# Optimization experiments

Measured on AMD Instinct MI355X. Metric: run time of the kernel, lower is better.

## Reference

```python
import jax, jax.numpy as jnp
import numpy as np

H_DIM = 4096
N_HEADS = 4
D_HEAD = H_DIM // N_HEADS  # 1024; also forced to equal the node count N
N = D_HEAD
LN_EPS = 1e-5


def setup_inputs() -> dict:
    key = jax.random.key(0)
    ks = jax.random.split(key, 10)
    s = 0.02
    return {
        "node1": jax.random.normal(ks[0], (N, H_DIM), dtype=jnp.float32),
        "node2": jax.random.normal(ks[1], (N, H_DIM), dtype=jnp.float32),
        # stacked per-head projection weights (torch Linear y = x @ W^T + b; here W stored as [h, in, out])
        "Wq": jax.random.normal(ks[2], (N_HEADS, H_DIM, D_HEAD), dtype=jnp.float32) * s,
        "bq": jax.random.normal(ks[3], (N_HEADS, D_HEAD), dtype=jnp.float32) * s,
        "Wk": jax.random.normal(ks[4], (N_HEADS, H_DIM, D_HEAD), dtype=jnp.float32) * s,
        "bk": jax.random.normal(ks[5], (N_HEADS, D_HEAD), dtype=jnp.float32) * s,
        "Wv": jax.random.normal(ks[6], (N_HEADS, H_DIM, D_HEAD), dtype=jnp.float32) * s,
        "bv": jax.random.normal(ks[7], (N_HEADS, D_HEAD), dtype=jnp.float32) * s,
        "gamma": jnp.ones((H_DIM,), dtype=jnp.float32),
        "beta": jnp.zeros((H_DIM,), dtype=jnp.float32),
    }


def reference(node1, node2, Wq, bq, Wk, bk, Wv, bv, gamma, beta):
    # per-head projections: [h, N, d]
    q = jnp.einsum('nd,hdf->hnf', node1, Wq) + bq[:, None, :]
    k = jnp.einsum('md,hdf->hmf', node2, Wk) + bk[:, None, :]
    v = jnp.einsum('md,hdf->hmf', node2, Wv) + bv[:, None, :]
    scale = 1.0 / jnp.sqrt(jnp.asarray(D_HEAD, dtype=q.dtype))
    # scores [h, N, N]; elementwise-multiplied by v (no softmax). Valid because N == D_HEAD.
    r = (jnp.einsum('hnf,hmf->hnm', q, k) * scale) * v
    # concat heads along last dim: [N, h * d] = [N, H_DIM]
    out = jnp.transpose(r, (1, 0, 2)).reshape(N, H_DIM)
    # LayerNorm over last dim (biased variance, matching torch)
    mu = jnp.mean(out, axis=-1, keepdims=True)
    var = jnp.mean((out - mu) ** 2, axis=-1, keepdims=True)
    return (out - mu) * jax.lax.rsqrt(var + LN_EPS) * gamma + beta
```

## Files before the change

### kernel.cpp

```cpp
#include <hip/hip_runtime.h>

#define H_DIM 4096
#define DH 1024
#define NROWS 1024

typedef __attribute__((ext_vector_type(8))) short short8;
typedef __attribute__((ext_vector_type(4))) short short4v;
typedef __attribute__((ext_vector_type(4))) float f32x4;

#define AS_GLOBAL __attribute__((address_space(1)))
#define AS_LDS __attribute__((address_space(3)))

__device__ __forceinline__ short f2bf(float f) {
  union { float f; unsigned u; } v; v.f = f;
  unsigned r = v.u + 0x7fffu + ((v.u >> 16) & 1u);
  return (short)(r >> 16);
}
__device__ __forceinline__ float bf2f(short s) {
  union { unsigned u; float f; } v;
  v.u = ((unsigned)(unsigned short)s) << 16;
  return v.f;
}

__device__ __forceinline__ void gload16(const void* g, void* l) {
  __builtin_amdgcn_global_load_lds((const AS_GLOBAL void*)g, (AS_LDS void*)l, 16, 0, 0);
}

__device__ __forceinline__ void stage_tile(const short* Xrow0, size_t rowstride, int kbase,
                                           short* lds, int t) {
  const int w = t >> 6;
#pragma unroll
  for (int p = 0; p < 2; ++p) {
    const short* g = Xrow0 + (size_t)(p * 64 + (t >> 2)) * rowstride + kbase + (t & 3) * 8;
    char* l = (char*)lds + p * 4096 + w * 1024;
    gload16(g, l);
  }
}

__global__ void convert_nodes(const float* __restrict__ n1, const float* __restrict__ n2,
                              short* __restrict__ o1, short* __restrict__ o2) {
  const float* src = blockIdx.y ? n2 : n1;
  short* dst = blockIdx.y ? o2 : o1;
  const size_t i = ((size_t)blockIdx.x * 256 + threadIdx.x) * 8;
  f32x4 a = *(const f32x4*)&src[i];
  f32x4 b = *(const f32x4*)&src[i + 4];
  short8 s;
  s[0] = f2bf(a.x); s[1] = f2bf(a.y); s[2] = f2bf(a.z); s[3] = f2bf(a.w);
  s[4] = f2bf(b.x); s[5] = f2bf(b.y); s[6] = f2bf(b.z); s[7] = f2bf(b.w);
  *(short8*)&dst[i] = s;
}

__global__ void convert_w_t(const float* __restrict__ W, short* __restrict__ Wt) {
  __shared__ short tile[64][72];
  const int h = blockIdx.z, dt = blockIdx.y, ft = blockIdx.x;
  const float* Wh = W + (size_t)h * H_DIM * DH;
  short* Wth = Wt + (size_t)h * DH * H_DIM;
  const int t = threadIdx.x;
  {
    const int d = t >> 2, f0 = (t & 3) * 16;
    const float* src = Wh + (size_t)(dt * 64 + d) * DH + ft * 64 + f0;
    f32x4 v0 = *(const f32x4*)(src + 0);
    f32x4 v1 = *(const f32x4*)(src + 4);
    f32x4 v2 = *(const f32x4*)(src + 8);
    f32x4 v3 = *(const f32x4*)(src + 12);
    short8 s0, s1;
    s0[0] = f2bf(v0.x); s0[1] = f2bf(v0.y); s0[2] = f2bf(v0.z); s0[3] = f2bf(v0.w);
    s0[4] = f2bf(v1.x); s0[5] = f2bf(v1.y); s0[6] = f2bf(v1.z); s0[7] = f2bf(v1.w);
    s1[0] = f2bf(v2.x); s1[1] = f2bf(v2.y); s1[2] = f2bf(v2.z); s1[3] = f2bf(v2.w);
    s1[4] = f2bf(v3.x); s1[5] = f2bf(v3.y); s1[6] = f2bf(v3.z); s1[7] = f2bf(v3.w);
    *(short8*)&tile[d][f0] = s0;
    *(short8*)&tile[d][f0 + 8] = s1;
  }
  __syncthreads();
  {
    const int f = t >> 2, d0 = (t & 3) * 16;
    short8 o0, o1;
#pragma unroll
    for (int j = 0; j < 8; ++j) o0[j] = tile[d0 + j][f];
#pragma unroll
    for (int j = 0; j < 8; ++j) o1[j] = tile[d0 + 8 + j][f];
    short* dst = Wth + (size_t)(ft * 64 + f) * H_DIM + dt * 64 + d0;
    *(short8*)(dst) = o0;
    *(short8*)(dst + 8) = o1;
  }
}

__launch_bounds__(256)
__global__ void qkv_bt(const short* __restrict__ n1b, const short* __restrict__ n2b,
                       const short* __restrict__ Wt,
                       const float* __restrict__ bq, const float* __restrict__ bk,
                       const float* __restrict__ bv,
                       short* __restrict__ qkv_out, int g0) {
  const int bid = blockIdx.x;
  const int gl = bid >> 6;
  const int gg = g0 + gl;
  const int tile = bid & 63;
  const short* A = (gg < 4) ? n1b : n2b;
  const short* B = Wt + (size_t)gl * NROWS * H_DIM;
  const float* bias = ((gg < 4) ? bq : (gg < 8) ? bk : bv) + (gg & 3) * DH;
  short* C = qkv_out + (size_t)gg * NROWS * DH;
  const int bm0 = (tile >> 3) * 128, bn0 = (tile & 7) * 128;

  __shared__ short As[2][4096];
  __shared__ short Bs[2][4096];

  const int t = threadIdx.x;
  const int lane = t & 63, w = t >> 6;
  const int wm = (w >> 1) * 64, wn = (w & 1) * 64;
  const int lr = lane & 15, lk = lane >> 4;

  const short* Arow0 = A + (size_t)bm0 * H_DIM;
  const short* Brow0 = B + (size_t)bn0 * H_DIM;

  f32x4 acc[4][4];
#pragma unroll
  for (int m = 0; m < 4; ++m)
#pragma unroll
    for (int n = 0; n < 4; ++n)
      acc[m][n] = (f32x4)(0.0f);

  stage_tile(Arow0, H_DIM, 0, &As[0][0], t);
  stage_tile(Brow0, H_DIM, 0, &Bs[0][0], t);
  __syncthreads();

  const int NKT = H_DIM / 32;
  int cur = 0;
  for (int kt = 0; kt < NKT; ++kt) {
    if (kt + 1 < NKT) {
      stage_tile(Arow0, H_DIM, (kt + 1) * 32, &As[cur ^ 1][0], t);
      stage_tile(Brow0, H_DIM, (kt + 1) * 32, &Bs[cur ^ 1][0], t);
    }
    short8 af[4], bf_[4];
#pragma unroll
    for (int m = 0; m < 4; ++m)
      af[m] = *(const short8*)((const char*)&As[cur][0] + (wm + m * 16 + lr) * 64 + lk * 16);
#pragma unroll
    for (int n = 0; n < 4; ++n)
      bf_[n] = *(const short8*)((const char*)&Bs[cur][0] + (wn + n * 16 + lr) * 64 + lk * 16);
#pragma unroll
    for (int m = 0; m < 4; ++m)
#pragma unroll
      for (int n = 0; n < 4; ++n)
        acc[m][n] = __builtin_amdgcn_mfma_f32_16x16x32_bf16(af[m], bf_[n], acc[m][n], 0, 0, 0);
    __syncthreads();
    cur ^= 1;
  }

#pragma unroll
  for (int n = 0; n < 4; ++n) {
    const int col = bn0 + wn + n * 16 + lr;
    const float bv_ = bias[col];
#pragma unroll
    for (int m = 0; m < 4; ++m) {
      const int row0 = bm0 + wm + m * 16 + lk * 4;
#pragma unroll
      for (int r = 0; r < 4; ++r)
        C[(size_t)(row0 + r) * DH + col] = f2bf(acc[m][n][r] + bv_);
    }
  }
}

__launch_bounds__(256)
__global__ void attn_bt(const short* __restrict__ qkv, float* __restrict__ out) {
  const int bid = blockIdx.x;
  const int h = bid >> 6;
  const int tile = bid & 63;
  const short* Q = qkv + (size_t)h * NROWS * DH;
  const short* K = qkv + (size_t)(4 + h) * NROWS * DH;
  const short* V = qkv + (size_t)(8 + h) * NROWS * DH;
  const int bm0 = (tile >> 3) * 128, bn0 = (tile & 7) * 128;

  __shared__ short As[2][4096];
  __shared__ short Bs[2][4096];

  const int t = threadIdx.x;
  const int lane = t & 63, w = t >> 6;
  const int wm = (w >> 1) * 64, wn = (w & 1) * 64;
  const int lr = lane & 15, lk = lane >> 4;

  const short* Arow0 = Q + (size_t)bm0 * DH;
  const short* Brow0 = K + (size_t)bn0 * DH;

  f32x4 acc[4][4];
#pragma unroll
  for (int m = 0; m < 4; ++m)
#pragma unroll
    for (int n = 0; n < 4; ++n)
      acc[m][n] = (f32x4)(0.0f);

  stage_tile(Arow0, DH, 0, &As[0][0], t);
  stage_tile(Brow0, DH, 0, &Bs[0][0], t);
  __syncthreads();

  const int NKT = DH / 32;
  int cur = 0;
  for (int kt = 0; kt < NKT; ++kt) {
    if (kt + 1 < NKT) {
      stage_tile(Arow0, DH, (kt + 1) * 32, &As[cur ^ 1][0], t);
      stage_tile(Brow0, DH, (kt + 1) * 32, &Bs[cur ^ 1][0], t);
    }
    short8 af[4], bf_[4];
#pragma unroll
    for (int m = 0; m < 4; ++m)
      af[m] = *(const short8*)((const char*)&As[cur][0] + (wm + m * 16 + lr) * 64 + lk * 16);
#pragma unroll
    for (int n = 0; n < 4; ++n)
      bf_[n] = *(const short8*)((const char*)&Bs[cur][0] + (wn + n * 16 + lr) * 64 + lk * 16);
#pragma unroll
    for (int m = 0; m < 4; ++m)
#pragma unroll
      for (int n = 0; n < 4; ++n)
        acc[m][n] = __builtin_amdgcn_mfma_f32_16x16x32_bf16(af[m], bf_[n], acc[m][n], 0, 0, 0);
    __syncthreads();
    cur ^= 1;
  }

  const float scale = 0.03125f;
#pragma unroll
  for (int n = 0; n < 4; ++n) {
    const int col = bn0 + wn + n * 16 + lr;
#pragma unroll
    for (int m = 0; m < 4; ++m) {
      const int row0 = bm0 + wm + m * 16 + lk * 4;
#pragma unroll
      for (int r = 0; r < 4; ++r) {
        const int row = row0 + r;
        const float vv = bf2f(V[(size_t)row * DH + col]);
        out[(size_t)row * H_DIM + h * DH + col] = acc[m][n][r] * scale * vv;
      }
    }
  }
}

__launch_bounds__(256, 2)
__global__ void qkv_gemm(const float* __restrict__ node1,
                         const float* __restrict__ node2,
                         const float* __restrict__ Wq, const float* __restrict__ bq,
                         const float* __restrict__ Wk, const float* __restrict__ bk,
                         const float* __restrict__ Wv, const float* __restrict__ bv,
                         short* __restrict__ qkv_out) {
  const int gid = blockIdx.x;
  const int gemm = gid >> 6;
  const int tile = gid & 63;
  const int qkv = gemm >> 2;
  const int h = gemm & 3;
  const float* A = (qkv == 0) ? node1 : node2;
  const float* W = (qkv == 0) ? Wq : (qkv == 1 ? Wk : Wv);
  const float* bias = (qkv == 0) ? bq : (qkv == 1 ? bk : bv);
  const float* B = W + (size_t)h * H_DIM * DH;
  const float* bh = bias + h * DH;
  short* C = qkv_out + (size_t)gemm * NROWS * DH;
  const int bm0 = (tile >> 3) * 128;
  const int bn0 = (tile & 7) * 128;
  __shared__ short As[128][40];
  __shared__ short Bs[128][40];
  const int t = threadIdx.x;
  const int lane = t & 63;
  const int w = t >> 6;
  const int wm = (w >> 1) * 64;
  const int wn = (w & 1) * 64;
  const int lr = lane & 15;
  const int lk = lane >> 4;
  const int ar = t >> 3;
  const int ac = (t & 7) * 4;
  const int bfc = t & 127;
  const int bd = (t >> 7) * 16;
  f32x4 acc[4][4];
#pragma unroll
  for (int m = 0; m < 4; ++m)
#pragma unroll
    for (int n = 0; n < 4; ++n)
      acc[m][n] = (f32x4)(0.0f);
  f32x4 rA[4];
  float rB[16];
  const float* Abase = A + (size_t)bm0 * H_DIM;
  const float* Bbase = B + bn0 + bfc;
#pragma unroll
  for (int p = 0; p < 4; ++p)
    rA[p] = *(const f32x4*)&Abase[(size_t)(ar + 32 * p) * H_DIM + ac];
#pragma unroll
  for (int i = 0; i < 16; ++i)
    rB[i] = Bbase[(size_t)(bd + i) * DH];
  const int NKT = H_DIM / 32;
  for (int kt = 0; kt < NKT; ++kt) {
    __syncthreads();
#pragma unroll
    for (int p = 0; p < 4; ++p) {
      short4v s;
      s.x = f2bf(rA[p].x); s.y = f2bf(rA[p].y);
      s.z = f2bf(rA[p].z); s.w = f2bf(rA[p].w);
      *(short4v*)&As[ar + 32 * p][ac] = s;
    }
    {
      short8 lo, hi;
#pragma unroll
      for (int i = 0; i < 8; ++i) { lo[i] = f2bf(rB[i]); hi[i] = f2bf(rB[8 + i]); }
      *(short8*)&Bs[bfc][bd] = lo;
      *(short8*)&Bs[bfc][bd + 8] = hi;
    }
    __syncthreads();
    if (kt + 1 < NKT) {
      const int k0 = (kt + 1) * 32;
#pragma unroll
      for (int p = 0; p < 4; ++p)
        rA[p] = *(const f32x4*)&Abase[(size_t)(ar + 32 * p) * H_DIM + k0 + ac];
#pragma unroll
      for (int i = 0; i < 16; ++i)
        rB[i] = Bbase[(size_t)(k0 + bd + i) * DH];
    }
    short8 af[4], bf_[4];
#pragma unroll
    for (int m = 0; m < 4; ++m)
      af[m] = *(const short8*)&As[wm + m * 16 + lr][lk * 8];
#pragma unroll
    for (int n = 0; n < 4; ++n)
      bf_[n] = *(const short8*)&Bs[wn + n * 16 + lr][lk * 8];
#pragma unroll
    for (int m = 0; m < 4; ++m)
#pragma unroll
      for (int n = 0; n < 4; ++n)
        acc[m][n] = __builtin_amdgcn_mfma_f32_16x16x32_bf16(af[m], bf_[n], acc[m][n], 0, 0, 0);
  }
#pragma unroll
  for (int n = 0; n < 4; ++n) {
    const int col = bn0 + wn + n * 16 + lr;
    const float bv_ = bh[col];
#pragma unroll
    for (int m = 0; m < 4; ++m) {
      const int row0 = bm0 + wm + m * 16 + lk * 4;
#pragma unroll
      for (int r = 0; r < 4; ++r)
        C[(size_t)(row0 + r) * DH + col] = f2bf(acc[m][n][r] + bv_);
    }
  }
}

__launch_bounds__(256, 4)
__global__ void ln_kernel(float* __restrict__ out, const float* __restrict__ gamma,
                          const float* __restrict__ beta) {
  const int row = blockIdx.x;
  const int t = threadIdx.x;
  float* p = out + (size_t)row * H_DIM;
  f32x4 x[4];
  float s1 = 0.f, s2 = 0.f;
#pragma unroll
  for (int i = 0; i < 4; ++i) {
    x[i] = *(const f32x4*)&p[t * 4 + i * 1024];
    s1 += x[i].x + x[i].y + x[i].z + x[i].w;
    s2 += x[i].x * x[i].x + x[i].y * x[i].y + x[i].z * x[i].z + x[i].w * x[i].w;
  }
#pragma unroll
  for (int o = 32; o > 0; o >>= 1) {
    s1 += __shfl_down(s1, o);
    s2 += __shfl_down(s2, o);
  }
  __shared__ float w1[4], w2[4];
  if ((t & 63) == 0) { w1[t >> 6] = s1; w2[t >> 6] = s2; }
  __syncthreads();
  const float tot1 = w1[0] + w1[1] + w1[2] + w1[3];
  const float tot2 = w2[0] + w2[1] + w2[2] + w2[3];
  const float mu = tot1 * (1.0f / H_DIM);
  const float var = tot2 * (1.0f / H_DIM) - mu * mu;
  const float rs = rsqrtf(var + 1e-5f);
#pragma unroll
  for (int i = 0; i < 4; ++i) {
    const int c = t * 4 + i * 1024;
    const f32x4 g = *(const f32x4*)&gamma[c];
    const f32x4 b = *(const f32x4*)&beta[c];
    f32x4 y;
    y.x = (x[i].x - mu) * rs * g.x + b.x;
    y.y = (x[i].y - mu) * rs * g.y + b.y;
    y.z = (x[i].z - mu) * rs * g.z + b.z;
    y.w = (x[i].w - mu) * rs * g.w + b.w;
    *(f32x4*)&p[c] = y;
  }
}

extern "C" void kernel_launch(void* const* d_in, const int* in_sizes, int n_in,
                              void* d_out, int out_size, void* d_ws, size_t ws_size,
                              hipStream_t stream) {
  const float* node1 = (const float*)d_in[0];
  const float* node2 = (const float*)d_in[1];
  const float* Wq = (const float*)d_in[2];
  const float* bq = (const float*)d_in[3];
  const float* Wk = (const float*)d_in[4];
  const float* bk = (const float*)d_in[5];
  const float* Wv = (const float*)d_in[6];
  const float* bv = (const float*)d_in[7];
  const float* gamma = (const float*)d_in[8];
  const float* beta = (const float*)d_in[9];
  float* out = (float*)d_out;

  const size_t MB = (size_t)1 << 20;
  short* qkv = (short*)d_ws;
  short* n1b = qkv + ((size_t)12 << 20);
  short* n2b = n1b + ((size_t)4 << 20);
  short* Wt = qkv + ((size_t)20 << 20);

  if (ws_size >= 136 * MB) {
    convert_nodes<<<dim3(2048, 2), 256, 0, stream>>>(node1, node2, n1b, n2b);
    convert_w_t<<<dim3(16, 64, 4), 256, 0, stream>>>(Wq, Wt);
    convert_w_t<<<dim3(16, 64, 4), 256, 0, stream>>>(Wk, Wt + ((size_t)16 << 20));
    convert_w_t<<<dim3(16, 64, 4), 256, 0, stream>>>(Wv, Wt + ((size_t)32 << 20));
    qkv_bt<<<768, 256, 0, stream>>>(n1b, n2b, Wt, bq, bk, bv, qkv, 0);
  } else if (ws_size >= 72 * MB) {
    convert_nodes<<<dim3(2048, 2), 256, 0, stream>>>(node1, node2, n1b, n2b);
    const float* Ws[3] = {Wq, Wk, Wv};
    for (int s = 0; s < 3; ++s) {
      convert_w_t<<<dim3(16, 64, 4), 256, 0, stream>>>(Ws[s], Wt);
      qkv_bt<<<256, 256, 0, stream>>>(n1b, n2b, Wt, bq, bk, bv, qkv, s * 4);
    }
  } else {
    qkv_gemm<<<768, 256, 0, stream>>>(node1, node2, Wq, bq, Wk, bk, Wv, bv, qkv);
  }

  attn_bt<<<256, 256, 0, stream>>>(qkv, out);
  ln_kernel<<<1024, 256, 0, stream>>>(out, gamma, beta);
}
```

Measured before the change: 237.6 us.

## Replace QKV GEMM with 256x256-tile 8-wave pipelined kernel using swizzled LDS

Replaces the 128x128-tile QKV projection GEMM with a kernel using 256x256 output tiles, 8 waves, and a BK=64 double-buffered LDS pipeline. LDS is XOR-swizzled, loads are interleaved with MFMA phases using barriers and s_setprio, and blocks are remapped across GEMMs. The aim is to raise arithmetic intensity per LDS byte and hide global load latency. It also drops the mid-workspace fallback path, so that size range now takes the slow fp32 GEMM, and 192 blocks of 512 threads may underfill the GPU's CUs.

```diff
diff --git a/kernel.cpp b/kernel.cpp
--- a/kernel.cpp
+++ b/kernel.cpp
@@ -24,17 +24,6 @@
 
 __device__ __forceinline__ void gload16(const void* g, void* l) {
   __builtin_amdgcn_global_load_lds((const AS_GLOBAL void*)g, (AS_LDS void*)l, 16, 0, 0);
-}
-
-__device__ __forceinline__ void stage_tile(const short* Xrow0, size_t rowstride, int kbase,
-                                           short* lds, int t) {
-  const int w = t >> 6;
-#pragma unroll
-  for (int p = 0; p < 2; ++p) {
-    const short* g = Xrow0 + (size_t)(p * 64 + (t >> 2)) * rowstride + kbase + (t & 3) * 8;
-    char* l = (char*)lds + p * 4096 + w * 1024;
-    gload16(g, l);
-  }
 }
 
 __global__ void convert_nodes(const float* __restrict__ n1, const float* __restrict__ n2,
@@ -85,78 +74,142 @@
   }
 }
 
-__launch_bounds__(256)
-__global__ void qkv_bt(const short* __restrict__ n1b, const short* __restrict__ n2b,
+
+#define BAR __builtin_amdgcn_s_barrier();
+#define WAITL { asm volatile("s_waitcnt lgkmcnt(0)" ::: "memory"); __builtin_amdgcn_sched_barrier(0); }
+#define PRIO1 __builtin_amdgcn_s_setprio(1);
+#define PRIO0 __builtin_amdgcn_s_setprio(0);
+
+#define STG(isA, slab, ktn) \
+  gload16(((isA) ? Ag : Bg) + (size_t)(slab) * 64 * H_DIM + (ktn) * 64, \
+          smb + ((isA) ? 0 : 65536) + ((ktn) & 1) * 32768 + (slab) * 8192 + wub)
+
+#define DSA(mh, cbuf) { _Pragma("unroll") for (int mp = 0; mp < 4; ++mp) { \
+    const int rrow = wm * 128 + (mh) * 64 + mp * 16 + lr; \
+    const char* pb = smb + (cbuf) * 32768 + rrow * 128; \
+    af[mp * 2 + 0] = *(const short8*)(pb + sA0); \
+    af[mp * 2 + 1] = *(const short8*)(pb + sA1); } }
+
+#define DSB(nh, cbuf, dst) { _Pragma("unroll") for (int np = 0; np < 2; ++np) { \
+    const int brow = wn * 64 + (nh) * 32 + np * 16 + lr; \
+    const char* pb = smb + 65536 + (cbuf) * 32768 + brow * 128; \
+    dst[np * 2 + 0] = *(const short8*)(pb + sA0); \
+    dst[np * 2 + 1] = *(const short8*)(pb + sA1); } }
+
+#define MFMA16(mh, nh, bfr) { _Pragma("unroll") for (int mp = 0; mp < 4; ++mp) \
+    { _Pragma("unroll") for (int np = 0; np < 2; ++np) { \
+      acc[(mh) * 4 + mp][(nh) * 2 + np] = __builtin_amdgcn_mfma_f32_16x16x32_bf16( \
+          af[mp * 2 + 0], bfr[np * 2 + 0], acc[(mh) * 4 + mp][(nh) * 2 + np], 0, 0, 0); \
+      acc[(mh) * 4 + mp][(nh) * 2 + np] = __builtin_amdgcn_mfma_f32_16x16x32_bf16( \
+          af[mp * 2 + 1], bfr[np * 2 + 1], acc[(mh) * 4 + mp][(nh) * 2 + np], 0, 0, 0); } } }
+
+__launch_bounds__(512, 2)
+__global__ void qkv_8p(const short* __restrict__ n1b, const short* __restrict__ n2b,
                        const short* __restrict__ Wt,
                        const float* __restrict__ bq, const float* __restrict__ bk,
                        const float* __restrict__ bv,
-                       short* __restrict__ qkv_out, int g0) {
+                       short* __restrict__ qkv_out) {
+  __shared__ short smem[65536];
+  char* smb = (char*)smem;
+
   const int bid = blockIdx.x;
-  const int gl = bid >> 6;
-  const int gg = g0 + gl;
-  const int tile = bid & 63;
-  const short* A = (gg < 4) ? n1b : n2b;
-  const short* B = Wt + (size_t)gl * NROWS * H_DIM;
-  const float* bias = ((gg < 4) ? bq : (gg < 8) ? bk : bv) + (gg & 3) * DH;
-  short* C = qkv_out + (size_t)gg * NROWS * DH;
-  const int bm0 = (tile >> 3) * 128, bn0 = (tile & 7) * 128;
-
-  __shared__ short As[2][4096];
-  __shared__ short Bs[2][4096];
+  const int v = (bid & 7) * 24 + (bid >> 3);
+  const int gemm = v >> 4;
+  const int rr = v & 15;
+  const int mt = rr & 3, nt = rr >> 2;
+  const int bm0 = mt * 256, bn0 = nt * 256;
+  const short* A = (gemm < 4) ? n1b : n2b;
+  const short* B = Wt + ((size_t)gemm << 22);
+  const float* bias = ((gemm < 4) ? bq : (gemm < 8) ? bk : bv) + (gemm & 3) * DH;
+  short* C = qkv_out + ((size_t)gemm << 20);
 
   const int t = threadIdx.x;
   const int lane = t & 63, w = t >> 6;
-  const int wm = (w >> 1) * 64, wn = (w & 1) * 64;
+  const int wm = w >> 2, wn = w & 3;
   const int lr = lane & 15, lk = lane >> 4;
-
-  const short* Arow0 = A + (size_t)bm0 * H_DIM;
-  const short* Brow0 = B + (size_t)bn0 * H_DIM;
-
-  f32x4 acc[4][4];
-#pragma unroll
-  for (int m = 0; m < 4; ++m)
+  const int xorv = lr & 7;
+  const int sA0 = (lk ^ xorv) * 16;
+  const int sA1 = ((4 + lk) ^ xorv) * 16;
+
+  const int rowA = t >> 3;
+  const int sL = (t & 7) ^ (rowA & 7);
+  const size_t wub = (size_t)w * 1024;
+  const short* Ag = A + (size_t)(bm0 + rowA) * H_DIM + sL * 8;
+  const short* Bg = B + (size_t)(bn0 + rowA) * H_DIM + sL * 8;
+
+  f32x4 acc[8][4];
+#pragma unroll
+  for (int m = 0; m < 8; ++m)
 #pragma unroll
     for (int n = 0; n < 4; ++n)
       acc[m][n] = (f32x4)(0.0f);
 
-  stage_tile(Arow0, H_DIM, 0, &As[0][0], t);
-  stage_tile(Brow0, H_DIM, 0, &Bs[0][0], t);
-  __syncthreads();
-
-  const int NKT = H_DIM / 32;
-  int cur = 0;
+  short8 af[8], bf0[4], bf1[4];
+
+#pragma unroll
+  for (int i = 0; i < 4; ++i) { STG(1, i, 0); }
+#pragma unroll
+  for (int i = 0; i < 4; ++i) { STG(0, i, 0); }
+#pragma unroll
+  for (int i = 0; i < 4; ++i) { STG(1, i, 1); }
+#pragma unroll
+  for (int i = 0; i < 4; ++i) { STG(0, i, 1); }
+
+  const int NKT = H_DIM / 64;
   for (int kt = 0; kt < NKT; ++kt) {
-    if (kt + 1 < NKT) {
-      stage_tile(Arow0, H_DIM, (kt + 1) * 32, &As[cur ^ 1][0], t);
-      stage_tile(Brow0, H_DIM, (kt + 1) * 32, &Bs[cur ^ 1][0], t);
-    }
-    short8 af[4], bf_[4];
-#pragma unroll
-    for (int m = 0; m < 4; ++m)
-      af[m] = *(const short8*)((const char*)&As[cur][0] + (wm + m * 16 + lr) * 64 + lk * 16);
-#pragma unroll
-    for (int n = 0; n < 4; ++n)
-      bf_[n] = *(const short8*)((const char*)&Bs[cur][0] + (wn + n * 16 + lr) * 64 + lk * 16);
-#pragma unroll
-    for (int m = 0; m < 4; ++m)
-#pragma unroll
-      for (int n = 0; n < 4; ++n)
-        acc[m][n] = __builtin_amdgcn_mfma_f32_16x16x32_bf16(af[m], bf_[n], acc[m][n], 0, 0, 0);
-    __syncthreads();
-    cur ^= 1;
-  }
-
-#pragma unroll
-  for (int n = 0; n < 4; ++n) {
-    const int col = bn0 + wn + n * 16 + lr;
-    const float bv_ = bias[col];
-#pragma unroll
-    for (int m = 0; m < 4; ++m) {
-      const int row0 = bm0 + wm + m * 16 + lk * 4;
-#pragma unroll
-      for (int r = 0; r < 4; ++r)
-        C[(size_t)(row0 + r) * DH + col] = f2bf(acc[m][n][r] + bv_);
-    }
+    const int cb = kt & 1;
+    if (kt == NKT - 1) { asm volatile("s_waitcnt vmcnt(0)" ::: "memory"); }
+    else               { asm volatile("s_waitcnt vmcnt(8)" ::: "memory"); }
+    BAR
+    DSA(0, cb)
+    DSB(0, cb, bf0)
+    BAR
+    WAITL
+    PRIO1 MFMA16(0, 0, bf0) PRIO0
+    BAR
+    const int dost = (kt + 2 < NKT);
+    if (dost) { STG(1, 0, kt + 2); STG(1, 2, kt + 2); }
+    DSB(1, cb, bf1)
+    BAR
+    WAITL
+    PRIO1 MFMA16(0, 1, bf1) PRIO0
+    BAR
+    if (dost) { STG(0, 0, kt + 2); STG(0, 1, kt + 2); }
+    DSA(1, cb)
+    BAR
+    WAITL
+    PRIO1 MFMA16(1, 1, bf1) PRIO0
+    BAR
+    if (dost) { STG(0, 2, kt + 2); STG(0, 3, kt + 2); STG(1, 1, kt + 2); STG(1, 3, kt + 2); }
+    BAR
+    PRIO1 MFMA16(1, 0, bf0) PRIO0
+    BAR
+  }
+
+  float bvv[4];
+#pragma unroll
+  for (int n = 0; n < 4; ++n) bvv[n] = bias[bn0 + wn * 64 + n * 16 + lr];
+#pragma unroll
+  for (int m = 0; m < 8; ++m) {
+    const int row0 = bm0 + wm * 128 + m * 16 + lk * 4;
+#pragma unroll
+    for (int n = 0; n < 4; ++n) {
+      const int col = bn0 + wn * 64 + n * 16 + lr;
+#pragma unroll
+      for (int e = 0; e < 4; ++e)
+        C[(size_t)(row0 + e) * DH + col] = f2bf(acc[m][n][e] + bvv[n]);
+    }
+  }
+}
+
+__device__ __forceinline__ void stage_tile(const short* Xrow0, size_t rowstride, int kbase,
+                                           short* lds, int t) {
+  const int w = t >> 6;
+#pragma unroll
+  for (int p = 0; p < 2; ++p) {
+    const short* g = Xrow0 + (size_t)(p * 64 + (t >> 2)) * rowstride + kbase + (t & 3) * 8;
+    char* l = (char*)lds + p * 4096 + w * 1024;
+    gload16(g, l);
   }
 }
 
@@ -402,14 +455,7 @@
     convert_w_t<<<dim3(16, 64, 4), 256, 0, stream>>>(Wq, Wt);
     convert_w_t<<<dim3(16, 64, 4), 256, 0, stream>>>(Wk, Wt + ((size_t)16 << 20));
     convert_w_t<<<dim3(16, 64, 4), 256, 0, stream>>>(Wv, Wt + ((size_t)32 << 20));
-    qkv_bt<<<768, 256, 0, stream>>>(n1b, n2b, Wt, bq, bk, bv, qkv, 0);
-  } else if (ws_size >= 72 * MB) {
-    convert_nodes<<<dim3(2048, 2), 256, 0, stream>>>(node1, node2, n1b, n2b);
-    const float* Ws[3] = {Wq, Wk, Wv};
-    for (int s = 0; s < 3; ++s) {
-      convert_w_t<<<dim3(16, 64, 4), 256, 0, stream>>>(Ws[s], Wt);
-      qkv_bt<<<256, 256, 0, stream>>>(n1b, n2b, Wt, bq, bk, bv, qkv, s * 4);
-    }
+    qkv_8p<<<192, 512, 0, stream>>>(n1b, n2b, Wt, bq, bk, bv, qkv);
   } else {
     qkv_gemm<<<768, 256, 0, stream>>>(node1, node2, Wq, bq, Wk, bk, Wv, bv, qkv);
   }
```

Measured after the change: 213.3 us. 10.3% less time.
